# Optimization experiments

Measured on AMD Instinct MI355X. Metric: run time of the kernel, lower is better.

The kernel has to match this reference:

```python
import jax, jax.numpy as jnp
import numpy as np

B, CIN, COUT, H, W = 4, 256, 256, 64, 64
EPS = 1e-5


def _conv1x1(x, w, b):
    # x: [B,C,H,W], w: [O,C], b: [O]
    return jnp.einsum('bchw,oc->bohw', x, w) + b[:, None, None]


def _conv3x3(x, w, b):
    y = jax.lax.conv_general_dilated(x, w, (1, 1), 'SAME',
                                     dimension_numbers=('NCHW', 'OIHW', 'NCHW'))
    return y + b[:, None, None]


def _bn(x, g, b, m, v):
    # inference-mode BatchNorm2d
    return g[:, None, None] * (x - m[:, None, None]) * jax.lax.rsqrt(v[:, None, None] + EPS) + b[:, None, None]


def setup_inputs():
    key = jax.random.key(0)
    keys = iter(jax.random.split(key, 64))
    nrm = lambda shape, s=0.05: jax.random.normal(next(keys), shape, dtype=jnp.float32) * s
    uni = lambda shape: jax.random.uniform(next(keys), shape, dtype=jnp.float32, minval=0.5, maxval=1.5)
    C, C2 = COUT, COUT // 2
    d = {}
    d['x'] = nrm((B, CIN, H, W), 1.0)
    d['wq'] = nrm((C2, CIN)); d['bq'] = nrm((C2,))
    d['wk'] = nrm((C2, CIN)); d['bk'] = nrm((C2,))
    d['wv'] = nrm((C, CIN)); d['bv'] = nrm((C,))
    d['d1_w'] = nrm((C, C)); d['d1_b'] = nrm((C,))
    for p in ['bn1', 'lbn1', 'lbn2', 'lbn3']:
        d[p + '_g'] = uni((C,)); d[p + '_b'] = nrm((C,))
        d[p + '_m'] = nrm((C,)); d[p + '_v'] = uni((C,))
    d['l1_w'] = nrm((C, C)); d['l1_b'] = nrm((C,))
    d['l2_w'] = nrm((C, C, 3, 3)); d['l2_b'] = nrm((C,))
    d['l3_w'] = nrm((C, C)); d['l3_b'] = nrm((C,))
    d['r1_w'] = nrm((C2, C)); d['r1_b'] = nrm((C2,))
    d['rbn_g'] = uni((C2,)); d['rbn_b'] = nrm((C2,))
    d['rbn_m'] = nrm((C2,)); d['rbn_v'] = uni((C2,))
    d['r2_w'] = nrm((C, C2)); d['r2_b'] = nrm((C,))
    return d


def _forward(x, wq, bq, wk, bk, wv, bv, d1_w, d1_b,
             bn1_g, bn1_b, bn1_m, bn1_v,
             l1_w, l1_b, lbn1_g, lbn1_b, lbn1_m, lbn1_v,
             l2_w, l2_b, lbn2_g, lbn2_b, lbn2_m, lbn2_v,
             l3_w, l3_b, lbn3_g, lbn3_b, lbn3_m, lbn3_v,
             r1_w, r1_b, rbn_g, rbn_b, rbn_m, rbn_v, r2_w, r2_b):
    b, _, h, w = x.shape
    n = h * w
    q = _conv1x1(x, wq, bq).reshape(b, -1, n)   # [B, C/2, N]
    k = _conv1x1(x, wk, bk).reshape(b, -1, n)   # [B, C/2, N]
    v = _conv1x1(x, wv, bv).reshape(b, -1, n)   # [B, C,   N]
    energy = jnp.einsum('bcn,bcm->bnm', q, k)   # [B, N, N] (query^T key)
    attn = jax.nn.softmax(energy, axis=-1)
    # feature = bmm(value, attn^T): feat[b,c,n] = sum_m v[b,c,m] * attn[b,n,m]
    feat = jnp.einsum('bcm,bnm->bcn', v, attn).reshape(b, -1, h, w)
    # dual1 gate: sigmoid(relu(bn(conv1x1(feat))))
    gate1 = jax.nn.sigmoid(jax.nn.relu(_bn(_conv1x1(feat, d1_w, d1_b), bn1_g, bn1_b, bn1_m, bn1_v)))
    y = feat * gate1
    # dual2_l: 1x1 -> 3x3 -> 1x1 conv/bn/relu stack
    yl = jax.nn.relu(_bn(_conv1x1(y, l1_w, l1_b), lbn1_g, lbn1_b, lbn1_m, lbn1_v))
    yl = jax.nn.relu(_bn(_conv3x3(yl, l2_w, l2_b), lbn2_g, lbn2_b, lbn2_m, lbn2_v))
    yl = jax.nn.relu(_bn(_conv1x1(yl, l3_w, l3_b), lbn3_g, lbn3_b, lbn3_m, lbn3_v))
    # dual2_r: global-avg-pool SE branch
    pooled = jnp.mean(y, axis=(2, 3), keepdims=True)  # [B, C, 1, 1]
    yr = jax.nn.relu(_bn(_conv1x1(pooled, r1_w, r1_b), rbn_g, rbn_b, rbn_m, rbn_v))
    yr = _conv1x1(yr, r2_w, r2_b)
    return feat * jax.nn.sigmoid(yl + yr)


def reference(x, wq, bq, wk, bk, wv, bv, d1_w, d1_b,
              bn1_g, bn1_b, bn1_m, bn1_v,
              l1_w, l1_b, lbn1_g, lbn1_b, lbn1_m, lbn1_v,
              l2_w, l2_b, lbn2_g, lbn2_b, lbn2_m, lbn2_v,
              l3_w, l3_b, lbn3_g, lbn3_b, lbn3_m, lbn3_v,
              r1_w, r1_b, rbn_g, rbn_b, rbn_m, rbn_v, r2_w, r2_b):
    return _forward(x, wq, bq, wk, bk, wv, bv, d1_w, d1_b,
                    bn1_g, bn1_b, bn1_m, bn1_v,
                    l1_w, l1_b, lbn1_g, lbn1_b, lbn1_m, lbn1_v,
                    l2_w, l2_b, lbn2_g, lbn2_b, lbn2_m, lbn2_v,
                    l3_w, l3_b, lbn3_g, lbn3_b, lbn3_m, lbn3_v,
                    r1_w, r1_b, rbn_g, rbn_b, rbn_m, rbn_v, r2_w, r2_b)
```

## Files before the change

### kernel.cpp

```cpp
#include <hip/hip_runtime.h>
#include <math.h>

#define NPIX 4096
#define EPSBN 1e-5f

typedef __attribute__((ext_vector_type(8))) short bf16x8;
typedef __attribute__((ext_vector_type(4))) float f32x4;

__device__ __forceinline__ float sigmoidf_(float x) { return 1.0f / (1.0f + expf(-x)); }

__device__ __forceinline__ short f2bf(float f) {
    unsigned u = __float_as_uint(f);
    u += 0x7fffu + ((u >> 16) & 1u);
    return (short)(u >> 16);
}
__device__ __forceinline__ float bf2f(short s) {
    return __uint_as_float(((unsigned)(unsigned short)s) << 16);
}
__device__ __forceinline__ int pk2(float lo, float hi) {
    return (int)(unsigned short)f2bf(lo) | ((int)(unsigned short)f2bf(hi) << 16);
}

__device__ __forceinline__ void gl_lds16(const short* g, short* l) {
    __builtin_amdgcn_global_load_lds(
        (const __attribute__((address_space(1))) void*)g,
        (__attribute__((address_space(3))) void*)l, 16, 0, 0);
}

template <int EPI, int BM, int BN>
__global__ __launch_bounds__(256) void gbt_k(
    const short* __restrict__ A, int lda,
    const short* __restrict__ B, int ldb,
    void* __restrict__ Cv, void* __restrict__ Cv2, int Ktot,
    const float* __restrict__ bias, const float* __restrict__ bias2,
    const float* __restrict__ bng, const float* __restrict__ bnb,
    const float* __restrict__ bnm, const float* __restrict__ bnv,
    const short* __restrict__ aux, const float* __restrict__ yrp)
{
    constexpr int FI = BM / 32, FJ = BN / 32;
    constexpr int SA = BM / 64, SB = BN / 64;
    __shared__ alignas(16) short lsA[2 * BM * 32];
    __shared__ alignas(16) short lsB[2 * BN * 32];

    const int tid = threadIdx.x;
    const int l = tid & 63;
    const int wv = tid >> 6;
    const int wm = wv >> 1, wn = wv & 1;
    const int m0 = blockIdx.y * BM;
    const int n0 = blockIdx.x * BN;

    const short* arow[2];
    const short* brow[2];
#pragma unroll
    for (int s = 0; s < SA; ++s) {
        int r = wv * (16 * SA) + s * 16 + (l >> 2);
        int sd = (l & 3) ^ ((r >> 1) & 3);
        if (EPI == 5) {
            int g = m0 + r;
            int p = (g >> 12) * 4356 + (((g & 4095) >> 6) + 1) * 66 + ((g & 63) + 1);
            arow[s] = A + (size_t)p * 256 + (sd << 3);
        } else {
            arow[s] = A + (size_t)(m0 + r) * lda + (sd << 3);
        }
    }
#pragma unroll
    for (int s = 0; s < SB; ++s) {
        int r = wv * (16 * SB) + s * 16 + (l >> 2);
        int sd = (l & 3) ^ ((r >> 1) & 3);
        brow[s] = B + (size_t)(n0 + r) * ldb + (sd << 3);
    }

    const int ks = l >> 4;
    const int lc = l & 15;
    int aoff[FI], boff[FJ];
#pragma unroll
    for (int f = 0; f < FI; ++f) {
        int ra = wm * (BM / 2) + f * 16 + lc;
        aoff[f] = ra * 64 + ((ks ^ ((ra >> 1) & 3)) << 4);
    }
#pragma unroll
    for (int f = 0; f < FJ; ++f) {
        int rb = wn * (BN / 2) + f * 16 + lc;
        boff[f] = rb * 64 + ((ks ^ ((rb >> 1) & 3)) << 4);
    }

    auto stage = [&](int d, int k0l) {
        int eA, eB;
        if (EPI == 5) {
            int t = k0l >> 8, ci0 = k0l & 255;
            eA = ((t / 3) * 66 + (t % 3) - 67) * 256 + ci0;
            eB = t * 65536 + ci0;
        } else if (EPI == 1) {
            eA = (k0l < 256) ? k0l : k0l - 256;
            eB = k0l;
        } else {
            eA = k0l; eB = k0l;
        }
        short* dA = lsA + d * (BM * 32) + wv * (SA * 512);
        short* dB = lsB + d * (BN * 32) + wv * (SB * 512);
#pragma unroll
        for (int s = 0; s < SA; ++s) gl_lds16(arow[s] + eA, dA + s * 512);
#pragma unroll
        for (int s = 0; s < SB; ++s) gl_lds16(brow[s] + eB, dB + s * 512);
    };

    f32x4 acc[FI][FJ] = {};
    const int nt = Ktot >> 5;

    stage(0, 0);
    __syncthreads();
    int cur = 0;
    for (int t = 0; t < nt; ++t) {
        if (t + 1 < nt) stage(cur ^ 1, (t + 1) << 5);
        bf16x8 af[FI], bfr[FJ];
#pragma unroll
        for (int f = 0; f < FI; ++f)
            af[f] = *(const bf16x8*)((const char*)lsA + cur * (BM * 64) + aoff[f]);
#pragma unroll
        for (int f = 0; f < FJ; ++f)
            bfr[f] = *(const bf16x8*)((const char*)lsB + cur * (BN * 64) + boff[f]);
#pragma unroll
        for (int i = 0; i < FI; ++i)
#pragma unroll
            for (int j = 0; j < FJ; ++j)
                acc[i][j] = __builtin_amdgcn_mfma_f32_16x16x32_bf16(af[i], bfr[j], acc[i][j], 0, 0, 0);
        __syncthreads();
        cur ^= 1;
    }

    float colsum[FJ < 1 ? 1 : FJ] = {};
    const int lr = (l >> 4) << 2;
#pragma unroll
    for (int i = 0; i < FI; ++i) {
        const int rowl = wm * (BM / 2) + i * 16 + lr;
#pragma unroll
        for (int j = 0; j < FJ; ++j) {
            const int coll = n0 + wn * (BN / 2) + j * 16 + lc;

            float sc = 0.f, tc = 0.f, bi = 0.f;
            if constexpr (EPI == 1) {
                bi = (coll < 128) ? bias[coll] : bias2[coll - 128];
            } else if constexpr (EPI == 3 || EPI == 4 || EPI == 5) {
                sc = bng[coll] * rsqrtf(bnv[coll] + EPSBN);
                tc = bnb[coll] - bnm[coll] * sc;
                bi = bias[coll];
            }

#pragma unroll
            for (int r = 0; r < 4; ++r) {
                const int row = m0 + rowl + r;
                float vvv = acc[i][j][r];
                if constexpr (EPI == 1) {
                    float val = vvv + bi;
                    short hi = f2bf(val);
                    short lo = f2bf(val - bf2f(hi));
                    size_t rb = (size_t)row * 256;
                    if (coll < 128) {
                        short* qb_ = (short*)Cv;
                        qb_[rb + coll] = hi;
                        qb_[rb + 128 + coll] = lo;
                    } else {
                        short* kb_ = (short*)Cv2;
                        int c = coll - 128;
                        kb_[rb + c] = hi;
                        kb_[rb + 128 + c] = lo;
                    }
                } else if constexpr (EPI == 2) {
                    int bb = coll >> 12;
                    ((short*)Cv)[((size_t)bb * 256 + row) * 4096 + (coll & 4095)] = f2bf(vvv + bias[row]);
                } else if constexpr (EPI == 3) {
                    float g = sigmoidf_(fmaxf(sc * (vvv + bi) + tc, 0.f));
                    float fv = bf2f(aux[(size_t)row * 256 + coll]);
                    float yv = fv * g;
                    ((short*)Cv)[(size_t)row * 256 + coll] = f2bf(yv);
                    colsum[j] += yv;
                } else if constexpr (EPI == 4) {
                    float rv = fmaxf(sc * (vvv + bi) + tc, 0.f);
                    int bb = row >> 12, n = row & 4095;
                    int pr = bb * 4356 + ((n >> 6) + 1) * 66 + (n & 63) + 1;
                    ((short*)Cv)[(size_t)pr * 256 + coll] = f2bf(rv);
                } else if constexpr (EPI == 5) {
                    float rv = fmaxf(sc * (vvv + bi) + tc, 0.f);
                    ((short*)Cv)[(size_t)row * 256 + coll] = f2bf(rv);
                } else if constexpr (EPI == 6) {
                    float s6 = bng[row] * rsqrtf(bnv[row] + EPSBN);
                    float t6 = bnb[row] - bnm[row] * s6;
                    int bb = coll >> 12;
                    float yl = fmaxf(s6 * (vvv + bias[row]) + t6, 0.f);
                    float sg = sigmoidf_(yl + yrp[bb * 256 + row]);
                    float fv = bf2f(aux[(size_t)coll * 256 + row]);
                    ((float*)Cv)[((size_t)bb * 256 + row) * 4096 + (coll & 4095)] = fv * sg;
                }
            }
        }
    }

    if constexpr (EPI == 3) {
        float* lsum = (float*)lsA;
#pragma unroll
        for (int j = 0; j < FJ; ++j) {
            int cl = wn * (BN / 2) + j * 16 + lc;
            lsum[cl * 8 + wm * 4 + ks] = colsum[j];
        }
        __syncthreads();
        if (tid < BN) {
            float s = 0.f;
#pragma unroll
            for (int u = 0; u < 8; ++u) s += lsum[tid * 8 + u];
            ((float*)Cv2)[(size_t)blockIdx.y * 256 + n0 + tid] = s;
        }
    }
}

__global__ __launch_bounds__(512, 2) void flash_k(
    const short* __restrict__ Q, const short* __restrict__ K,
    const short* __restrict__ V, short* __restrict__ Op, float* __restrict__ lp)
{
    __shared__ alignas(16) short smem[32768];

    const int tid = threadIdx.x;
    const int l = tid & 63;
    const int wv = tid >> 6;
    const int bid = blockIdx.x;
    const int combo = bid & 15;
    const int batch = combo >> 2;
    const int kvq = combo & 3;
    const int q0 = (bid >> 4) * 256;
    const int kv0 = kvq * 1024;

    const short* Qb = Q + (size_t)batch * 4096 * 256;
    const short* Kb = K + (size_t)batch * 4096 * 256;
    const short* Vb = V + (size_t)batch * 256 * 4096;

    const int lc = l & 15, ks = l >> 4;

    bf16x8 bq[2][8];
#pragma unroll
    for (int f = 0; f < 2; ++f)
#pragma unroll
        for (int cc = 0; cc < 8; ++cc)
            bq[f][cc] = *(const bf16x8*)(Qb +
                (size_t)(q0 + wv * 32 + f * 16 + lc) * 256 + cc * 32 + ks * 8);

    const short* ksrc[2]; short* kdst[2];
    const short* vsrc[2]; short* vdst[2];
#pragma unroll
    for (int i = 0; i < 2; ++i) {
        int slot = wv * 4 + i * 2 + (l >> 5);
        int grow = ((slot >> 2) & 3) * 8 + (slot >> 4) * 4 + (slot & 3);
        int s = l & 31;
        int g = s ^ (slot & 7);
        ksrc[i] = Kb + (size_t)(kv0 + grow) * 256 + g * 8;
        kdst[i] = smem + wv * 1024 + i * 512;
        int c = wv * 32 + i * 16 + (l >> 2);
        int sv = l & 3;
        int gv = sv ^ ((c >> 1) & 3);
        vsrc[i] = Vb + (size_t)c * 4096 + kv0 + gv * 8;
        vdst[i] = smem + 16384 + wv * 1024 + i * 512;
    }
    auto stageKV = [&](int buf, int t) {
#pragma unroll
        for (int i = 0; i < 2; ++i) gl_lds16(ksrc[i] + (size_t)t * 8192, kdst[i] + buf * 8192);
#pragma unroll
        for (int i = 0; i < 2; ++i) gl_lds16(vsrc[i] + t * 32, vdst[i] + buf * 8192);
    };

    stageKV(0, 0);
    __syncthreads();

    const int kro = lc * 512;
    const int kxr = lc & 7;
    const int vb0 = lc * 64 + ((ks ^ ((lc >> 1) & 3)) << 4);

    bf16x8 ones;
#pragma unroll
    for (int e = 0; e < 8; ++e) ones[e] = (short)0x3F80;

    f32x4 acc_o[2][16] = {};
    f32x4 acc_l[2] = {};

    int cur = 0;
    for (int t = 0; t < 32; ++t) {
        if (t + 1 < 32) stageKV(cur ^ 1, t + 1);

        const char* kb_ = (const char*)smem + cur * 16384;
        f32x4 s00 = {}, s01 = {}, s10 = {}, s11 = {};
        __builtin_amdgcn_s_setprio(1);
#pragma unroll
        for (int jc = 0; jc < 4; ++jc) {
#pragma unroll
            for (int kvf = 0; kvf < 2; ++kvf) {
                const char* rb_ = kb_ + kro + kvf * 8192;
                bf16x8 kh_ = *(const bf16x8*)(rb_ + ((((jc * 4) + ks) ^ kxr) << 4));
                bf16x8 kl_ = *(const bf16x8*)(rb_ + (((((jc + 4) * 4) + ks) ^ kxr) << 4));
                f32x4& sA = kvf ? s01 : s00;
                f32x4& sB = kvf ? s11 : s10;
                sA = __builtin_amdgcn_mfma_f32_16x16x32_bf16(kh_, bq[0][jc], sA, 0, 0, 0);
                sB = __builtin_amdgcn_mfma_f32_16x16x32_bf16(kh_, bq[1][jc], sB, 0, 0, 0);
                sA = __builtin_amdgcn_mfma_f32_16x16x32_bf16(kl_, bq[0][jc], sA, 0, 0, 0);
                sB = __builtin_amdgcn_mfma_f32_16x16x32_bf16(kl_, bq[1][jc], sB, 0, 0, 0);
                sA = __builtin_amdgcn_mfma_f32_16x16x32_bf16(kh_, bq[0][jc + 4], sA, 0, 0, 0);
                sB = __builtin_amdgcn_mfma_f32_16x16x32_bf16(kh_, bq[1][jc + 4], sB, 0, 0, 0);
            }
        }
        __builtin_amdgcn_s_setprio(0);

        bf16x8 pa[2];
#pragma unroll
        for (int f = 0; f < 2; ++f) {
            const f32x4& sa = f ? s10 : s00;
            const f32x4& sb = f ? s11 : s01;
            union { int i4[4]; bf16x8 v; } un;
            un.i4[0] = pk2(__expf(sa[0]), __expf(sa[1]));
            un.i4[1] = pk2(__expf(sa[2]), __expf(sa[3]));
            un.i4[2] = pk2(__expf(sb[0]), __expf(sb[1]));
            un.i4[3] = pk2(__expf(sb[2]), __expf(sb[3]));
            pa[f] = un.v;
        }

        const char* vbb = (const char*)smem + 32768 + cur * 16384;
        __builtin_amdgcn_s_setprio(1);
#pragma unroll
        for (int j = 0; j < 16; ++j) {
            bf16x8 vv = *(const bf16x8*)(vbb + vb0 + j * 1024);
            acc_o[0][j] = __builtin_amdgcn_mfma_f32_16x16x32_bf16(pa[0], vv, acc_o[0][j], 0, 0, 0);
            acc_o[1][j] = __builtin_amdgcn_mfma_f32_16x16x32_bf16(pa[1], vv, acc_o[1][j], 0, 0, 0);
        }
        acc_l[0] = __builtin_amdgcn_mfma_f32_16x16x32_bf16(pa[0], ones, acc_l[0], 0, 0, 0);
        acc_l[1] = __builtin_amdgcn_mfma_f32_16x16x32_bf16(pa[1], ones, acc_l[1], 0, 0, 0);
        __builtin_amdgcn_s_setprio(0);
        __syncthreads();
        cur ^= 1;
    }

    short* Ob = Op + ((size_t)combo * 4096 + q0 + wv * 32) * 256;
#pragma unroll
    for (int f = 0; f < 2; ++f)
#pragma unroll
        for (int j = 0; j < 16; ++j)
#pragma unroll
            for (int r = 0; r < 4; ++r)
                Ob[(size_t)(f * 16 + ks * 4 + r) * 256 + j * 16 + lc] = f2bf(acc_o[f][j][r]);
    if (lc == 0) {
        float* lb = lp + (size_t)combo * 4096 + q0 + wv * 32;
#pragma unroll
        for (int f = 0; f < 2; ++f)
#pragma unroll
            for (int r = 0; r < 4; ++r)
                lb[f * 16 + ks * 4 + r] = acc_l[f][r];
    }
}

__global__ __launch_bounds__(256) void combine_k(const short* __restrict__ Op,
                                                 const float* __restrict__ lp,
                                                 short* __restrict__ o)
{
    int idx = blockIdx.x * 256 + threadIdx.x;
    size_t e = (size_t)idx * 4;
    int row = (int)(e >> 8);
    int batch = row >> 12, ql = row & 4095;
    int c = (int)(e & 255);
    size_t lbase = (size_t)batch * 4 * 4096 + ql;
    float li = 1.0f / (lp[lbase] + lp[lbase + 4096] + lp[lbase + 8192] + lp[lbase + 12288]);
    size_t base = ((size_t)(batch * 4) * 4096 + ql) * 256 + c;
    const short4 a = *(const short4*)(Op + base);
    const short4 b = *(const short4*)(Op + base + 1048576);
    const short4 cc = *(const short4*)(Op + base + 2097152);
    const short4 d = *(const short4*)(Op + base + 3145728);
    short4 o4;
    o4.x = f2bf((bf2f(a.x) + bf2f(b.x) + bf2f(cc.x) + bf2f(d.x)) * li);
    o4.y = f2bf((bf2f(a.y) + bf2f(b.y) + bf2f(cc.y) + bf2f(d.y)) * li);
    o4.z = f2bf((bf2f(a.z) + bf2f(b.z) + bf2f(cc.z) + bf2f(d.z)) * li);
    o4.w = f2bf((bf2f(a.w) + bf2f(b.w) + bf2f(cc.w) + bf2f(d.w)) * li);
    *(short4*)(o + (size_t)row * 256 + c) = o4;
}

__global__ __launch_bounds__(256) void transpose_x_k(const float* __restrict__ x,
                                                     short* __restrict__ xT2)
{
    __shared__ float t[64][65];
    const int b = blockIdx.z, c0 = blockIdx.y * 64, n0 = blockIdx.x * 64;
    const int tid = threadIdx.x;
#pragma unroll
    for (int rep = 0; rep < 16; ++rep) {
        int idx = tid + rep * 256;
        int i = idx >> 6, j = idx & 63;
        t[i][j] = x[((size_t)(b * 256 + c0 + i)) * NPIX + n0 + j];
    }
    __syncthreads();
#pragma unroll
    for (int rep = 0; rep < 16; ++rep) {
        int idx = tid + rep * 256;
        int i = idx >> 6, j = idx & 63;
        float v = t[j][i];
        short hi = f2bf(v);
        short lo = f2bf(v - bf2f(hi));
        size_t rb = ((size_t)(b * NPIX + n0 + i)) * 512;
        xT2[rb + c0 + j] = hi;
        xT2[rb + 256 + c0 + j] = lo;
    }
}

__global__ __launch_bounds__(256) void prep_k(
    const float* __restrict__ wq, const float* __restrict__ wk,
    const float* __restrict__ wvp, const float* __restrict__ d1w,
    const float* __restrict__ l1w, const float* __restrict__ l3w,
    const float* __restrict__ l2w,
    short* __restrict__ wqk3, short* __restrict__ wvb, short* __restrict__ d1wb,
    short* __restrict__ l1wb, short* __restrict__ l3wb, short* __restrict__ w2b)
{
    const int b = blockIdx.x;
    const int tid = threadIdx.x;
    if (b < 256) {
        int idx = b * 256 + tid;
        int o = idx >> 8, c = idx & 255;
        const float* src = (o < 128) ? wq : wk;
        float v = src[(o & 127) * 256 + c];
        short hi = f2bf(v);
        short lo = f2bf(v - bf2f(hi));
        size_t rb = (size_t)o * 768;
        wqk3[rb + c] = hi;
        wqk3[rb + 256 + c] = lo;
        wqk3[rb + 512 + c] = hi;
    } else if (b < 1280) {
        int g = (b - 256) >> 8;
        int i = ((b - 256) & 255) * 256 + tid;
        const float* s = g == 0 ? wvp : g == 1 ? d1w : g == 2 ? l1w : l3w;
        short* d = g == 0 ? wvb : g == 1 ? d1wb : g == 2 ? l1wb : l3wb;
        d[i] = f2bf(s[i]);
    } else {
        int idx = (b - 1280) * 256 + tid;
        int t = idx >> 16;
        int rem = idx & 65535;
        int co = rem >> 8, ci = rem & 255;
        w2b[idx] = f2bf(l2w[((size_t)(co * 256 + ci)) * 9 + t]);
    }
}

__global__ __launch_bounds__(256) void pool_s2_k(const float* __restrict__ pp2,
                                                 float* __restrict__ pooled)
{
    const int b = blockIdx.x;
    const int c = threadIdx.x;
    float s = 0.f;
#pragma unroll
    for (int k = 0; k < 32; ++k)
        s += pp2[(size_t)(b * 32 + k) * 256 + c];
    pooled[b * 256 + c] = s * (1.0f / NPIX);
}

__global__ __launch_bounds__(256) void se_k(
    const float* __restrict__ pooled,
    const float* __restrict__ r1w, const float* __restrict__ r1b,
    const float* __restrict__ g, const float* __restrict__ bb,
    const float* __restrict__ m, const float* __restrict__ vv,
    const float* __restrict__ r2w, const float* __restrict__ r2b,
    float* __restrict__ yr)
{
    const int b = blockIdx.x;
    const int tid = threadIdx.x;
    __shared__ float p[256], hbuf[128];
    p[tid] = pooled[b * 256 + tid];
    __syncthreads();
    if (tid < 128) {
        float a = r1b[tid];
        for (int ci = 0; ci < 256; ++ci) a = fmaf(r1w[tid * 256 + ci], p[ci], a);
        float s = g[tid] * rsqrtf(vv[tid] + EPSBN);
        float t = bb[tid] - m[tid] * s;
        hbuf[tid] = fmaxf(s * a + t, 0.f);
    }
    __syncthreads();
    float a = r2b[tid];
    for (int c2 = 0; c2 < 128; ++c2) a = fmaf(r2w[tid * 128 + c2], hbuf[c2], a);
    yr[b * 256 + tid] = a;
}

extern "C" void kernel_launch(void* const* d_in, const int* in_sizes, int n_in,
                              void* d_out, int out_size, void* d_ws, size_t ws_size,
                              hipStream_t stream)
{
    const float* x    = (const float*)d_in[0];
    const float* wq   = (const float*)d_in[1];
    const float* bq   = (const float*)d_in[2];
    const float* wk   = (const float*)d_in[3];
    const float* bk   = (const float*)d_in[4];
    const float* wvp  = (const float*)d_in[5];
    const float* bv   = (const float*)d_in[6];
    const float* d1w  = (const float*)d_in[7];
    const float* d1b  = (const float*)d_in[8];
    const float* bn1g = (const float*)d_in[9];
    const float* bn1b = (const float*)d_in[10];
    const float* bn1m = (const float*)d_in[11];
    const float* bn1v = (const float*)d_in[12];
    const float* lbn1g = (const float*)d_in[13];
    const float* lbn1b = (const float*)d_in[14];
    const float* lbn1m = (const float*)d_in[15];
    const float* lbn1v = (const float*)d_in[16];
    const float* lbn2g = (const float*)d_in[17];
    const float* lbn2b = (const float*)d_in[18];
    const float* lbn2m = (const float*)d_in[19];
    const float* lbn2v = (const float*)d_in[20];
    const float* lbn3g = (const float*)d_in[21];
    const float* lbn3b = (const float*)d_in[22];
    const float* lbn3m = (const float*)d_in[23];
    const float* lbn3v = (const float*)d_in[24];
    const float* l1w  = (const float*)d_in[25];
    const float* l1b  = (const float*)d_in[26];
    const float* l2w  = (const float*)d_in[27];
    const float* l2b  = (const float*)d_in[28];
    const float* l3w  = (const float*)d_in[29];
    const float* l3b  = (const float*)d_in[30];
    const float* r1w  = (const float*)d_in[31];
    const float* r1b  = (const float*)d_in[32];
    const float* rbng = (const float*)d_in[33];
    const float* rbnb = (const float*)d_in[34];
    const float* rbnm = (const float*)d_in[35];
    const float* rbnv = (const float*)d_in[36];
    const float* r2w  = (const float*)d_in[37];
    const float* r2b  = (const float*)d_in[38];

    float* out = (float*)d_out;
    char* wsb = (char*)d_ws;

    short* xT2  = (short*)(wsb);
    short* qbuf = (short*)(wsb + (24ull << 20));
    short* kbuf = (short*)(wsb + (32ull << 20));
    short* vbuf = (short*)(wsb + (40ull << 20));
    short* Opart= (short*)(wsb + (48ull << 20));
    short* featT= (short*)(wsb + (112ull << 20));
    float* lpart= (float*)(wsb + (120ull << 20));
    short* yT   = (short*)(wsb + (48ull << 20));
    short* t1pad= (short*)(wsb + (56ull << 20));
    short* t2T  = (short*)(wsb + (65ull << 20));
    short* wqk3 = (short*)(wsb + (121ull << 20));
    short* wvb  = wqk3 + 196608;
    short* d1wb = wvb + 65536;
    short* l1wb = d1wb + 65536;
    short* l3wb = l1wb + 65536;
    short* w2b  = l3wb + 65536;
    float* pooled = (float*)(wsb + (123ull << 20) + (512ull << 10));
    float* yrb  = pooled + 1024;
    float* ppart2 = yrb + 1024;

    dim3 blk(256);

    transpose_x_k<<<dim3(64, 4, 4), blk, 0, stream>>>(x, xT2);
    prep_k<<<3584, blk, 0, stream>>>(wq, wk, wvp, d1w, l1w, l3w, l2w,
                                     wqk3, wvb, d1wb, l1wb, l3wb, w2b);

    gbt_k<1, 128, 64><<<dim3(4, 128), blk, 0, stream>>>(xT2, 512, wqk3, 768, qbuf, kbuf, 768,
        bq, bk, nullptr, nullptr, nullptr, nullptr, nullptr, nullptr);
    gbt_k<2, 64, 128><<<dim3(128, 4), blk, 0, stream>>>(wvb, 256, xT2, 512, vbuf, nullptr, 256,
        bv, nullptr, nullptr, nullptr, nullptr, nullptr, nullptr, nullptr);

    flash_k<<<256, dim3(512), 0, stream>>>(qbuf, kbuf, vbuf, Opart, lpart);
    combine_k<<<4096, blk, 0, stream>>>(Opart, lpart, featT);

    gbt_k<3, 128, 64><<<dim3(4, 128), blk, 0, stream>>>(featT, 256, d1wb, 256, yT, ppart2, 256,
        d1b, nullptr, bn1g, bn1b, bn1m, bn1v, featT, nullptr);

    hipMemsetAsync(t1pad, 0, (size_t)4 * 4356 * 256 * 2, stream);

    pool_s2_k<<<4, blk, 0, stream>>>(ppart2, pooled);
    se_k<<<4, blk, 0, stream>>>(pooled, r1w, r1b, rbng, rbnb, rbnm, rbnv, r2w, r2b, yrb);

    gbt_k<4, 128, 64><<<dim3(4, 128), blk, 0, stream>>>(yT, 256, l1wb, 256, t1pad, nullptr, 256,
        l1b, nullptr, lbn1g, lbn1b, lbn1m, lbn1v, nullptr, nullptr);
    gbt_k<5, 128, 64><<<dim3(4, 128), blk, 0, stream>>>(t1pad, 256, w2b, 256, t2T, nullptr, 2304,
        l2b, nullptr, lbn2g, lbn2b, lbn2m, lbn2v, nullptr, nullptr);

    gbt_k<6, 64, 128><<<dim3(128, 4), blk, 0, stream>>>(l3wb, 256, t2T, 256, out, nullptr, 256,
        l3b, nullptr, lbn3g, lbn3b, lbn3m, lbn3v, featT, yrb);
}
```

Baseline: 224.6 us.

## Split flash attention KV range into eight chunks and fuse pooling into SE kernel

The attention kernel now splits each batch's key/value sequence into eight 512-wide chunks instead of four 1024-wide ones. That doubles the grid to 512 blocks, so with two blocks per CU the GPU gets more resident waves to hide latency. The combine kernel now sums eight partial outputs and denominators, doubling the partial-output traffic it reads and writes. Separately, the global-average-pool reduction is folded into the SE kernel, removing one tiny launch and its intermediate buffer.

```diff
diff --git a/kernel.cpp b/kernel.cpp
--- a/kernel.cpp
+++ b/kernel.cpp
@@ -222,11 +222,11 @@
     const int l = tid & 63;
     const int wv = tid >> 6;
     const int bid = blockIdx.x;
-    const int combo = bid & 15;
-    const int batch = combo >> 2;
-    const int kvq = combo & 3;
-    const int q0 = (bid >> 4) * 256;
-    const int kv0 = kvq * 1024;
+    const int combo = bid & 31;
+    const int batch = combo >> 3;
+    const int kvo = combo & 7;
+    const int q0 = (bid >> 5) * 256;
+    const int kv0 = kvo * 512;
 
     const short* Qb = Q + (size_t)batch * 4096 * 256;
     const short* Kb = K + (size_t)batch * 4096 * 256;
@@ -280,8 +280,8 @@
     f32x4 acc_l[2] = {};
 
     int cur = 0;
-    for (int t = 0; t < 32; ++t) {
-        if (t + 1 < 32) stageKV(cur ^ 1, t + 1);
+    for (int t = 0; t < 16; ++t) {
+        if (t + 1 < 16) stageKV(cur ^ 1, t + 1);
 
         const char* kb_ = (const char*)smem + cur * 16384;
         f32x4 s00 = {}, s01 = {}, s10 = {}, s11 = {};
@@ -360,18 +360,23 @@
     int row = (int)(e >> 8);
     int batch = row >> 12, ql = row & 4095;
     int c = (int)(e & 255);
-    size_t lbase = (size_t)batch * 4 * 4096 + ql;
-    float li = 1.0f / (lp[lbase] + lp[lbase + 4096] + lp[lbase + 8192] + lp[lbase + 12288]);
-    size_t base = ((size_t)(batch * 4) * 4096 + ql) * 256 + c;
-    const short4 a = *(const short4*)(Op + base);
-    const short4 b = *(const short4*)(Op + base + 1048576);
-    const short4 cc = *(const short4*)(Op + base + 2097152);
-    const short4 d = *(const short4*)(Op + base + 3145728);
+    size_t lbase = (size_t)batch * 8 * 4096 + ql;
+    float lsum = 0.f;
+#pragma unroll
+    for (int k = 0; k < 8; ++k) lsum += lp[lbase + (size_t)k * 4096];
+    float li = 1.0f / lsum;
+    size_t base = ((size_t)(batch * 8) * 4096 + ql) * 256 + c;
+    float s0 = 0.f, s1 = 0.f, s2 = 0.f, s3 = 0.f;
+#pragma unroll
+    for (int k = 0; k < 8; ++k) {
+        const short4 a = *(const short4*)(Op + base + (size_t)k * 1048576);
+        s0 += bf2f(a.x); s1 += bf2f(a.y); s2 += bf2f(a.z); s3 += bf2f(a.w);
+    }
     short4 o4;
-    o4.x = f2bf((bf2f(a.x) + bf2f(b.x) + bf2f(cc.x) + bf2f(d.x)) * li);
-    o4.y = f2bf((bf2f(a.y) + bf2f(b.y) + bf2f(cc.y) + bf2f(d.y)) * li);
-    o4.z = f2bf((bf2f(a.z) + bf2f(b.z) + bf2f(cc.z) + bf2f(d.z)) * li);
-    o4.w = f2bf((bf2f(a.w) + bf2f(b.w) + bf2f(cc.w) + bf2f(d.w)) * li);
+    o4.x = f2bf(s0 * li);
+    o4.y = f2bf(s1 * li);
+    o4.z = f2bf(s2 * li);
+    o4.w = f2bf(s3 * li);
     *(short4*)(o + (size_t)row * 256 + c) = o4;
 }
 
@@ -437,20 +442,8 @@
     }
 }
 
-__global__ __launch_bounds__(256) void pool_s2_k(const float* __restrict__ pp2,
-                                                 float* __restrict__ pooled)
-{
-    const int b = blockIdx.x;
-    const int c = threadIdx.x;
-    float s = 0.f;
-#pragma unroll
-    for (int k = 0; k < 32; ++k)
-        s += pp2[(size_t)(b * 32 + k) * 256 + c];
-    pooled[b * 256 + c] = s * (1.0f / NPIX);
-}
-
 __global__ __launch_bounds__(256) void se_k(
-    const float* __restrict__ pooled,
+    const float* __restrict__ pp2,
     const float* __restrict__ r1w, const float* __restrict__ r1b,
     const float* __restrict__ g, const float* __restrict__ bb,
     const float* __restrict__ m, const float* __restrict__ vv,
@@ -460,7 +453,11 @@
     const int b = blockIdx.x;
     const int tid = threadIdx.x;
     __shared__ float p[256], hbuf[128];
-    p[tid] = pooled[b * 256 + tid];
+    float s0 = 0.f;
+#pragma unroll
+    for (int k = 0; k < 32; ++k)
+        s0 += pp2[(size_t)(b * 32 + k) * 256 + tid];
+    p[tid] = s0 * (1.0f / NPIX);
     __syncthreads();
     if (tid < 128) {
         float a = r1b[tid];
@@ -538,8 +535,7 @@
     short* l1wb = d1wb + 65536;
     short* l3wb = l1wb + 65536;
     short* w2b  = l3wb + 65536;
-    float* pooled = (float*)(wsb + (123ull << 20) + (512ull << 10));
-    float* yrb  = pooled + 1024;
+    float* yrb  = (float*)(wsb + (123ull << 20) + (512ull << 10));
     float* ppart2 = yrb + 1024;
 
     dim3 blk(256);
@@ -553,7 +549,7 @@
     gbt_k<2, 64, 128><<<dim3(128, 4), blk, 0, stream>>>(wvb, 256, xT2, 512, vbuf, nullptr, 256,
         bv, nullptr, nullptr, nullptr, nullptr, nullptr, nullptr, nullptr);
 
-    flash_k<<<256, dim3(512), 0, stream>>>(qbuf, kbuf, vbuf, Opart, lpart);
+    flash_k<<<512, dim3(512), 0, stream>>>(qbuf, kbuf, vbuf, Opart, lpart);
     combine_k<<<4096, blk, 0, stream>>>(Opart, lpart, featT);
 
     gbt_k<3, 128, 64><<<dim3(4, 128), blk, 0, stream>>>(featT, 256, d1wb, 256, yT, ppart2, 256,
@@ -561,8 +557,7 @@
 
     hipMemsetAsync(t1pad, 0, (size_t)4 * 4356 * 256 * 2, stream);
 
-    pool_s2_k<<<4, blk, 0, stream>>>(ppart2, pooled);
-    se_k<<<4, blk, 0, stream>>>(pooled, r1w, r1b, rbng, rbnb, rbnm, rbnv, r2w, r2b, yrb);
+    se_k<<<4, blk, 0, stream>>>(ppart2, r1w, r1b, rbng, rbnb, rbnm, rbnv, r2w, r2b, yrb);
 
     gbt_k<4, 128, 64><<<dim3(4, 128), blk, 0, stream>>>(yT, 256, l1wb, 256, t1pad, nullptr, 256,
         l1b, nullptr, lbn1g, lbn1b, lbn1m, lbn1v, nullptr, nullptr);
```

Result: slower. 239.9 us (+6.8%).
